# Performance work log

Measured on AMD Instinct MI355X. Metric: run time of the kernel, lower is better.

The kernel has to match this reference:

```python
import jax, jax.numpy as jnp
import numpy as np

NEG_SLOPE = 0.1
NUM_HEADS = 16
ATT0, ATT1 = 64, 64
FOCUS = 3

def lrelu(x):
    return jnp.where(x >= 0, x, NEG_SLOPE * x)

def adaptive_pool_sum(x, a0, a1):
    # adaptive max pool + adaptive avg pool (exact windows since h%a0==0, w%a1==0)
    B, C, h, w = x.shape
    f0, f1 = h // a0, w // a1
    xr = x.reshape(B, C, a0, f0, a1, f1)
    return xr.max(axis=(3, 5)) + xr.mean(axis=(3, 5))

def upsample_bilinear_ac(x, H, W):
    # bilinear upsample with align_corners=True, matching nn.Upsample
    B, C, h, w = x.shape
    def grid(n_out, n_in):
        t = jnp.arange(n_out, dtype=x.dtype) * ((n_in - 1) / (n_out - 1))
        i0 = jnp.clip(jnp.floor(t).astype(jnp.int32), 0, n_in - 2)
        return i0, t - i0.astype(x.dtype)
    y0, wy = grid(H, h)
    x0, wx = grid(W, w)
    wy = wy[None, None, :, None]
    r = x[:, :, y0, :] * (1 - wy) + x[:, :, y0 + 1, :] * wy
    return r[:, :, :, x0] * (1 - wx) + r[:, :, :, x0 + 1] * wx

def _forward(input1, input2, w_in, b_in, w_v, b_v, scale_param, pos1, pos2):
    B, C, W, H = input1.shape
    N = ATT0 * ATT1
    HD = C // NUM_HEADS
    # conv2input: 1x1 conv dim//2 -> dim (channels differ)
    input2 = jnp.einsum('oc,bchw->bohw', w_in, input2) + b_in[None, :, None, None]
    p1 = adaptive_pool_sum(input1, ATT0, ATT1)  # (B,C,64,64)
    p2 = adaptive_pool_sum(input2, ATT0, ATT1)
    q = p1.reshape(B, C, N).transpose(0, 2, 1)  # (B,N,C)
    t2 = p2.reshape(B, C, N).transpose(0, 2, 1)
    q = lrelu(q + pos1)
    k = lrelu(t2 + pos2)
    v = t2
    scale = jax.nn.softplus(scale_param)  # (1,1,C)
    q = q / scale
    k = k / scale
    def focus(t):
        n = jnp.linalg.norm(t, axis=-1, keepdims=True)
        tp = t ** FOCUS
        return n / jnp.linalg.norm(tp, axis=-1, keepdims=True) * tp
    q = focus(q)
    k = focus(k)
    # head split is head-major: C -> (num_heads, head_dim)
    qh = q.reshape(B, N, NUM_HEADS, HD).transpose(0, 2, 1, 3)  # (B,h,N,d)
    kh = k.reshape(B, N, NUM_HEADS, HD).transpose(0, 2, 1, 3)
    vh = v.reshape(B, N, NUM_HEADS, HD).transpose(0, 2, 1, 3)
    # kv-first linear attention: (k^T N^-.5) @ (v N^-.5) = k^T v / N
    kv = jnp.einsum('bhnd,bhne->bhde', kh, vh) / N  # (B,h,d,d)
    x = jnp.einsum('bhnd,bhde->bhne', qh, kv)       # (B,h,N,d)
    x = x.transpose(0, 1, 3, 2).reshape(B, C, N)     # (B,h,d,N) -> (B,C,N)
    # per-head 1x1 conv + leaky relu on v
    v4 = vh.reshape(B * NUM_HEADS, ATT0, ATT1, HD)
    vc = lrelu(jnp.einsum('bxyd,od->boxy', v4, w_v) + b_v[None, :, None, None])
    x = x + vc.reshape(B, C, N)
    attn = x.reshape(B, C, ATT0, ATT1)
    attn = upsample_bilinear_ac(attn, W, H)
    return jax.nn.sigmoid(attn)

def setup_inputs():
    key = jax.random.key(0)
    ks = jax.random.split(key, 6)
    dim, half, hd, N = 512, 256, 32, ATT0 * ATT1
    return {
        'input1': jax.random.normal(ks[0], (8, dim, 128, 128), jnp.float32),
        'input2': jax.random.normal(ks[1], (8, half, 128, 128), jnp.float32),
        'w_in': jax.random.normal(ks[2], (dim, half), jnp.float32) * 0.05,
        'b_in': jnp.zeros((dim,), jnp.float32),
        'w_v': jax.random.normal(ks[3], (hd, hd), jnp.float32) * 0.1,
        'b_v': jnp.zeros((hd,), jnp.float32),
        'scale_param': jnp.zeros((1, 1, dim), jnp.float32),  # nn.Parameter init zeros
        'pos1': jax.random.normal(ks[4], (1, N, dim), jnp.float32) * 0.02,
        'pos2': jax.random.normal(ks[5], (1, N, dim), jnp.float32) * 0.02,
    }

def reference(input1, input2, w_in, b_in, w_v, b_v, scale_param, pos1, pos2):
    return _forward(input1, input2, w_in, b_in, w_v, b_v, scale_param, pos1, pos2)
```

## Files before the change

kernel.cpp:

```cpp
#include <hip/hip_runtime.h>
#include <hip/hip_bf16.h>
#include <math.h>

#define NEG 0.1f

typedef __attribute__((ext_vector_type(8))) short short8;
typedef __attribute__((ext_vector_type(4))) float f32x4;

__device__ __forceinline__ float lrelu(float x){ return x >= 0.f ? x : NEG*x; }

__device__ __forceinline__ unsigned pk2(float lo, float hi){
    __hip_bfloat162 h = __float22bfloat162_rn(make_float2(lo, hi));
    union { __hip_bfloat162 h2; unsigned u; } cv; cv.h2 = h;
    return cv.u;
}
__device__ __forceinline__ float bflo(unsigned u){ return __uint_as_float(u << 16); }
__device__ __forceinline__ float bfhi(unsigned u){ return __uint_as_float(u & 0xFFFF0000u); }

__global__ __launch_bounds__(256) void k_wprep(const float* __restrict__ w_in, unsigned* __restrict__ wbf_u){
    int idx8 = (blockIdx.x*256 + threadIdx.x)*8;
    float4 v0 = *(const float4*)&w_in[idx8];
    float4 v1 = *(const float4*)&w_in[idx8+4];
    uint4 d;
    d.x = pk2(v0.x, v0.y); d.y = pk2(v0.z, v0.w);
    d.z = pk2(v1.x, v1.y); d.w = pk2(v1.z, v1.w);
    *(uint4*)&wbf_u[idx8>>1] = d;
}

__global__ __launch_bounds__(256) void k_pool1(const float* __restrict__ in1, unsigned* __restrict__ p1u){
    const int y = blockIdx.x, cg = blockIdx.y, b = blockIdx.z;
    const int tid = threadIdx.x;
    const int x = tid & 63, w = tid >> 6;
    const int cbase = cg*32 + w*8;
    const float2* iv = (const float2*)in1;
    float out[8];
    #pragma unroll
    for (int j = 0; j < 8; ++j){
        int c = cbase + j;
        size_t r0 = (size_t)(b*512 + c)*8192 + (2*y)*64 + x;
        float2 a = iv[r0];
        float2 bb = iv[r0 + 64];
        float m = fmaxf(fmaxf(a.x,a.y), fmaxf(bb.x,bb.y));
        out[j] = m + (a.x+a.y+bb.x+bb.y)*0.25f;
    }
    uint4 d;
    d.x = pk2(out[0],out[1]); d.y = pk2(out[2],out[3]);
    d.z = pk2(out[4],out[5]); d.w = pk2(out[6],out[7]);
    int n = y*64 + x;
    *(uint4*)&p1u[(size_t)(b*4096 + n)*256 + cg*16 + w*4] = d;
}

__global__ __launch_bounds__(256) void k_convpool(const float* __restrict__ in2, const unsigned* __restrict__ wbf_u,
                                                  const float* __restrict__ b_in, unsigned short* __restrict__ p2t){
    __shared__ unsigned As[128*33];
    __shared__ unsigned Bs[128*32];
    const int b = blockIdx.z, o0 = blockIdx.y*128;
    const int y = blockIdx.x >> 1, xg = blockIdx.x & 1;
    const int tid = threadIdx.x;
    const int lane = tid & 63, w = tid >> 6;
    const int col = lane & 15, q = lane >> 4;

    f32x4 acc[2][8];
    #pragma unroll
    for (int mt=0; mt<2; ++mt)
        #pragma unroll
        for (int nt=0; nt<8; ++nt) acc[mt][nt] = (f32x4){0.f,0.f,0.f,0.f};

    const int a_o8 = tid >> 3;
    const int a_kg = tid & 7;
    const int b_c4 = tid & 15, b_r = (tid>>4)&1, b_kg = tid>>5;
    const int b_n = b_r*64 + b_c4*4;

    for (int kb = 0; kb < 4; ++kb){
        __syncthreads();
        #pragma unroll
        for (int pass=0; pass<4; ++pass){
            int o = pass*32 + a_o8;
            uint4 d = *(const uint4*)&wbf_u[((size_t)(o0+o)*256 + kb*64 + a_kg*8) >> 1];
            *(uint4*)&As[o*32 + ((a_kg ^ ((o>>1)&7))<<2)] = d;
        }
        float r[8][4];
        #pragma unroll
        for (int kk=0; kk<8; ++kk){
            int k = kb*64 + b_kg*8 + kk;
            float4 v = *(const float4*)&in2[((size_t)(b*256 + k)*128 + 2*y + b_r)*128 + xg*64 + b_c4*4];
            r[kk][0]=v.x; r[kk][1]=v.y; r[kk][2]=v.z; r[kk][3]=v.w;
        }
        #pragma unroll
        for (int i=0; i<4; ++i){
            int n = b_n + i;
            uint4 d;
            d.x = pk2(r[0][i], r[1][i]); d.y = pk2(r[2][i], r[3][i]);
            d.z = pk2(r[4][i], r[5][i]); d.w = pk2(r[6][i], r[7][i]);
            *(uint4*)&Bs[n*32 + ((b_kg ^ ((n>>1)&7))<<2)] = d;
        }
        __syncthreads();
        #pragma unroll
        for (int ks=0; ks<2; ++ks){
            int g = ks*4 + q;
            short8 af[2], bf[8];
            #pragma unroll
            for (int mt=0; mt<2; ++mt){
                int m = w*32 + mt*16 + col;
                af[mt] = *(const short8*)&As[m*32 + ((g ^ ((m>>1)&7))<<2)];
            }
            #pragma unroll
            for (int nt=0; nt<8; ++nt){
                int n = nt*16 + col;
                bf[nt] = *(const short8*)&Bs[n*32 + ((g ^ ((n>>1)&7))<<2)];
            }
            #pragma unroll
            for (int mt=0; mt<2; ++mt)
                #pragma unroll
                for (int nt=0; nt<8; ++nt)
                    acc[mt][nt] = __builtin_amdgcn_mfma_f32_16x16x32_bf16(af[mt], bf[nt], acc[mt][nt], 0,0,0);
        }
    }
    __syncthreads();
    float* outs = (float*)As;
    #pragma unroll
    for (int mt=0; mt<2; ++mt){
        #pragma unroll
        for (int nt=0; nt<4; ++nt){
            #pragma unroll
            for (int reg=0; reg<4; ++reg){
                float a = acc[mt][nt][reg], bb = acc[mt][nt+4][reg];
                float mx = fmaxf(a, bb), sm = a + bb;
                float mx2 = fmaxf(mx, __shfl_xor(mx, 1));
                float sm2 = sm + __shfl_xor(sm, 1);
                if ((lane & 1) == 0){
                    int p = nt*8 + (col>>1);
                    int o = w*32 + mt*16 + q*4 + reg;
                    outs[o*33 + p] = mx2 + sm2*0.25f;
                }
            }
        }
    }
    __syncthreads();
    const int o4 = tid & 31, pp = tid >> 5;
    #pragma unroll
    for (int pass=0; pass<4; ++pass){
        int p = pass*8 + pp;
        int n = y*64 + xg*32 + p;
        float v0 = outs[(o4*4+0)*33 + p] + 2.0f*b_in[o0+o4*4+0];
        float v1 = outs[(o4*4+1)*33 + p] + 2.0f*b_in[o0+o4*4+1];
        float v2 = outs[(o4*4+2)*33 + p] + 2.0f*b_in[o0+o4*4+2];
        float v3 = outs[(o4*4+3)*33 + p] + 2.0f*b_in[o0+o4*4+3];
        uint2 d; d.x = pk2(v0,v1); d.y = pk2(v2,v3);
        *(uint2*)&p2t[(size_t)(b*4096 + n)*512 + o0 + o4*4] = d;
    }
}

__global__ __launch_bounds__(256) void k_rows(unsigned* __restrict__ p1u, const unsigned* __restrict__ p2u,
                                              const float* __restrict__ pos1, const float* __restrict__ pos2,
                                              const float* __restrict__ scale_param, unsigned* __restrict__ kfu){
    const int b = blockIdx.y;
    const int tid = threadIdx.x;
    const int half = tid >> 7, t = tid & 127;
    const int n = blockIdx.x*2 + half;
    const int c0 = t*4;
    const size_t base2 = (size_t)(b*4096 + n)*128;
    __shared__ float red[4][4];
    uint2 u1 = *(const uint2*)&p1u[base2*2 + t*2];
    uint2 u2 = *(const uint2*)&p2u[base2*2 + t*2];
    float4 po1 = *(const float4*)&pos1[n*512 + c0];
    float4 po2 = *(const float4*)&pos2[n*512 + c0];
    float4 scv = *(const float4*)&scale_param[c0];
    float qv[4], kv_[4];
    float pq2=0.f, pq6=0.f, pk2_=0.f, pk6=0.f;
    {
        float p1a[4] = {bflo(u1.x), bfhi(u1.x), bflo(u1.y), bfhi(u1.y)};
        float p2a[4] = {bflo(u2.x), bfhi(u2.x), bflo(u2.y), bfhi(u2.y)};
        float poa1[4] = {po1.x,po1.y,po1.z,po1.w};
        float poa2[4] = {po2.x,po2.y,po2.z,po2.w};
        float sca[4] = {scv.x,scv.y,scv.z,scv.w};
        #pragma unroll
        for (int j = 0; j < 4; ++j){
            float sp = sca[j];
            float inv = 1.0f/(fmaxf(sp,0.f) + log1pf(expf(-fabsf(sp))));
            float qq = lrelu(p1a[j] + poa1[j]) * inv;
            float kk = lrelu(p2a[j] + poa2[j]) * inv;
            qv[j]=qq; kv_[j]=kk;
            float a;
            a = qq*qq; pq2 += a; pq6 += a*a*a;
            a = kk*kk; pk2_ += a; pk6 += a*a*a;
        }
    }
    #pragma unroll
    for (int off = 32; off > 0; off >>= 1){
        pq2 += __shfl_xor(pq2, off);
        pq6 += __shfl_xor(pq6, off);
        pk2_ += __shfl_xor(pk2_, off);
        pk6 += __shfl_xor(pk6, off);
    }
    int wave = tid >> 6;
    if ((tid & 63) == 0){ red[wave][0]=pq2; red[wave][1]=pq6; red[wave][2]=pk2_; red[wave][3]=pk6; }
    __syncthreads();
    float sq2 = red[2*half][0]+red[2*half+1][0];
    float sq6 = red[2*half][1]+red[2*half+1][1];
    float sk2 = red[2*half][2]+red[2*half+1][2];
    float sk6 = red[2*half][3]+red[2*half+1][3];
    float fq = sqrtf(sq2/sq6);
    float fk = sqrtf(sk2/sk6);
    uint2 dq, dk;
    dq.x = pk2(qv[0]*qv[0]*qv[0]*fq, qv[1]*qv[1]*qv[1]*fq);
    dq.y = pk2(qv[2]*qv[2]*qv[2]*fq, qv[3]*qv[3]*qv[3]*fq);
    dk.x = pk2(kv_[0]*kv_[0]*kv_[0]*fk, kv_[1]*kv_[1]*kv_[1]*fk);
    dk.y = pk2(kv_[2]*kv_[2]*kv_[2]*fk, kv_[3]*kv_[3]*kv_[3]*fk);
    *(uint2*)&p1u[base2*2 + t*2] = dq;
    *(uint2*)&kfu[base2*2 + t*2] = dk;
}

__global__ __launch_bounds__(256) void k_kv(const unsigned* __restrict__ kfu, const unsigned* __restrict__ p2u,
                                            float* __restrict__ kv){
    __shared__ unsigned ksu[4096], vsu[4096];
    const int nc = blockIdx.x, h = blockIdx.y, b = blockIdx.z;
    const int tid = threadIdx.x;
    #pragma unroll
    for (int it = 0; it < 16; ++it){
        int i = it*256 + tid;
        int n = i >> 4, u = i & 15;
        size_t g = (size_t)(b*4096 + nc*256 + n)*256 + h*16 + u;
        ksu[i] = kfu[g];
        vsu[i] = p2u[g];
    }
    __syncthreads();
    const int d = tid >> 3, e2 = (tid & 7)*2;
    const unsigned kmaskhi = (d & 1) ? 1u : 0u;
    float acc[4] = {0.f,0.f,0.f,0.f};
    #pragma unroll 8
    for (int n = 0; n < 256; ++n){
        unsigned ku = ksu[n*16 + (d>>1)];
        float kd = kmaskhi ? bfhi(ku) : bflo(ku);
        uint2 vv = *(const uint2*)&vsu[n*16 + e2];
        acc[0] += kd*bflo(vv.x); acc[1] += kd*bfhi(vv.x);
        acc[2] += kd*bflo(vv.y); acc[3] += kd*bfhi(vv.y);
    }
    float* dst = &kv[((size_t)(b*16 + h)*32 + d)*32 + (tid&7)*4];
    const float sc = 1.0f/4096.0f;
    atomicAdd(dst+0, acc[0]*sc);
    atomicAdd(dst+1, acc[1]*sc);
    atomicAdd(dst+2, acc[2]*sc);
    atomicAdd(dst+3, acc[3]*sc);
}

__global__ __launch_bounds__(256) void k_attn(const unsigned* __restrict__ qfu, const unsigned* __restrict__ p2u,
                                              const float* __restrict__ kv, const float* __restrict__ w_v,
                                              const float* __restrict__ b_v, unsigned short* __restrict__ attn){
    __shared__ float kvs[1024];
    __shared__ float wvsT[32*36];
    __shared__ float qsl[64*32];
    __shared__ float vsl[64*32];
    __shared__ float to[32*66];
    const int nt = blockIdx.x, h = blockIdx.y, b = blockIdx.z;
    const int tid = threadIdx.x;
    #pragma unroll
    for (int it = 0; it < 4; ++it){
        int i = it*256 + tid;
        kvs[i] = kv[(size_t)(b*16 + h)*1024 + i];
        int e_ = i >> 5, d_ = i & 31;
        wvsT[d_*36 + e_] = w_v[e_*32 + d_];
    }
    #pragma unroll
    for (int it = 0; it < 4; ++it){
        int i = it*256 + tid;
        int nn = i >> 4, cp = i & 15;
        size_t g = (size_t)(b*4096 + nt*64 + nn)*256 + h*16 + cp;
        unsigned qu = qfu[g], vu = p2u[g];
        qsl[nn*32 + cp*2]   = bflo(qu);
        qsl[nn*32 + cp*2+1] = bfhi(qu);
        vsl[nn*32 + cp*2]   = bflo(vu);
        vsl[nn*32 + cp*2+1] = bfhi(vu);
    }
    __syncthreads();
    const int e0 = (tid & 7)*4, ng = tid >> 3;
    float4 bv = make_float4(b_v[e0], b_v[e0+1], b_v[e0+2], b_v[e0+3]);
    #pragma unroll
    for (int half = 0; half < 2; ++half){
        int nn = ng + half*32;
        float xa[4] = {0.f,0.f,0.f,0.f}, va[4] = {0.f,0.f,0.f,0.f};
        #pragma unroll
        for (int dq = 0; dq < 8; ++dq){
            float4 q4 = *(const float4*)&qsl[nn*32 + dq*4];
            float4 v4 = *(const float4*)&vsl[nn*32 + dq*4];
            float qarr[4] = {q4.x,q4.y,q4.z,q4.w};
            float varr[4] = {v4.x,v4.y,v4.z,v4.w};
            #pragma unroll
            for (int l = 0; l < 4; ++l){
                int d = dq*4 + l;
                float4 kvv = *(const float4*)&kvs[d*32 + e0];
                float4 wvv = *(const float4*)&wvsT[d*36 + e0];
                xa[0] += qarr[l]*kvv.x; xa[1] += qarr[l]*kvv.y; xa[2] += qarr[l]*kvv.z; xa[3] += qarr[l]*kvv.w;
                va[0] += varr[l]*wvv.x; va[1] += varr[l]*wvv.y; va[2] += varr[l]*wvv.z; va[3] += varr[l]*wvv.w;
            }
        }
        to[(e0+0)*66 + nn] = xa[0] + lrelu(va[0] + bv.x);
        to[(e0+1)*66 + nn] = xa[1] + lrelu(va[1] + bv.y);
        to[(e0+2)*66 + nn] = xa[2] + lrelu(va[2] + bv.z);
        to[(e0+3)*66 + nn] = xa[3] + lrelu(va[3] + bv.w);
    }
    __syncthreads();
    const int cc = tid >> 3, n0 = (tid & 7)*8;
    uint4 d;
    d.x = pk2(to[cc*66+n0+0], to[cc*66+n0+1]);
    d.y = pk2(to[cc*66+n0+2], to[cc*66+n0+3]);
    d.z = pk2(to[cc*66+n0+4], to[cc*66+n0+5]);
    d.w = pk2(to[cc*66+n0+6], to[cc*66+n0+7]);
    *(uint4*)&attn[((size_t)(b*512) + h*32 + cc)*4096 + nt*64 + n0] = d;
}

__global__ __launch_bounds__(256) void k_up(const unsigned* __restrict__ attn_u, float* __restrict__ out){
    __shared__ float sA[18*65];
    const int qy = blockIdx.x;
    const int bc = blockIdx.y;
    const int tid = threadIdx.x;
    const int ybase = (qy*32*63)/127;
    const size_t sb = (size_t)bc*2048;
    for (int i = tid; i < 576; i += 256){
        int r = i >> 5, cu = i & 31;
        int ridx = ybase + r; if (ridx > 63) ridx = 63;
        unsigned u = attn_u[sb + ridx*32 + cu];
        sA[r*65 + cu*2]   = bflo(u);
        sA[r*65 + cu*2+1] = bfhi(u);
    }
    __syncthreads();
    const float rr = 63.0f/127.0f;
    const int ro = tid >> 3, cbase = tid & 7;
    const int yo = qy*32 + ro;
    float ty = yo * rr;
    int y0 = (int)ty; y0 = y0 > 62 ? 62 : y0;
    float wy = ty - (float)y0;
    const float* ra = &sA[(y0 - ybase)*65];
    const float* rb = ra + 65;
    float* orow = &out[((size_t)bc*128 + yo)*128];
    #pragma unroll
    for (int t = 0; t < 4; ++t){
        int xo0 = (cbase + t*8)*4;
        float4 o;
        float* op = (float*)&o;
        #pragma unroll
        for (int j = 0; j < 4; ++j){
            int xo = xo0 + j;
            float tx = xo * rr;
            int x0 = (int)tx; x0 = x0 > 62 ? 62 : x0;
            float wx = tx - (float)x0;
            float a00 = ra[x0], a01 = ra[x0+1];
            float a10 = rb[x0], a11 = rb[x0+1];
            float v = (a00*(1.f-wy) + a10*wy)*(1.f-wx) + (a01*(1.f-wy) + a11*wy)*wx;
            op[j] = 1.0f/(1.0f + expf(-v));
        }
        *(float4*)&orow[xo0] = o;
    }
}

extern "C" void kernel_launch(void* const* d_in, const int* in_sizes, int n_in,
                              void* d_out, int out_size, void* d_ws, size_t ws_size,
                              hipStream_t stream){
    const float* in1  = (const float*)d_in[0];
    const float* in2  = (const float*)d_in[1];
    const float* w_in = (const float*)d_in[2];
    const float* b_in = (const float*)d_in[3];
    const float* w_v  = (const float*)d_in[4];
    const float* b_v  = (const float*)d_in[5];
    const float* scp  = (const float*)d_in[6];
    const float* pos1 = (const float*)d_in[7];
    const float* pos2 = (const float*)d_in[8];
    float* out = (float*)d_out;
    char* ws  = (char*)d_ws;

    const size_t PBYTES = (size_t)8*4096*512*2;
    unsigned short* p1t  = (unsigned short*)ws;
    unsigned short* p2t  = (unsigned short*)(ws + PBYTES);
    unsigned short* kfoc = (unsigned short*)(ws + 2*PBYTES);
    float*          kvb  = (float*)(ws + 3*PBYTES);
    unsigned*       wbf  = (unsigned*)(ws + 3*PBYTES + (size_t)8*16*32*32*4);

    hipMemsetAsync(kvb, 0, (size_t)8*16*32*32*sizeof(float), stream);
    k_wprep   <<<64,            256, 0, stream>>>(w_in, wbf);
    k_pool1   <<<dim3(64,16,8), 256, 0, stream>>>(in1, (unsigned*)p1t);
    k_convpool<<<dim3(128,4,8), 256, 0, stream>>>(in2, wbf, b_in, p2t);
    k_rows    <<<dim3(2048,8),  256, 0, stream>>>((unsigned*)p1t, (const unsigned*)p2t, pos1, pos2, scp, (unsigned*)kfoc);
    k_kv      <<<dim3(16,16,8), 256, 0, stream>>>((const unsigned*)kfoc, (const unsigned*)p2t, kvb);
    k_attn    <<<dim3(64,16,8), 256, 0, stream>>>((const unsigned*)p1t, (const unsigned*)p2t, kvb, w_v, b_v, kfoc);
    k_up      <<<dim3(4,4096),  256, 0, stream>>>((const unsigned*)kfoc, out);
}
```

Measured before the change: 813.2 us.

## Use MFMA with split-bf16 in attention, register-tile kv, coalesce pool1 stores

k_attn now does the q·kv and v·w_v products with bf16 MFMA instructions. kv and w_v are split into high and low bf16 parts so that precision stays close to fp32 while scalar FMA loops are removed. k_kv gives each thread a 4x4 register tile, spreads the rows across waves, reduces the partials in shared memory, and processes 1024 rows per block. That cuts the number of atomics and the LDS traffic per multiply-add. k_pool1 now stages its outputs in shared memory so the bf16 stores are contiguous, at the cost of an extra barrier.

Result: faster. 742.6 us (-8.7%).

```diff
diff --git a/kernel.cpp b/kernel.cpp
--- a/kernel.cpp
+++ b/kernel.cpp
@@ -16,6 +16,11 @@
 }
 __device__ __forceinline__ float bflo(unsigned u){ return __uint_as_float(u << 16); }
 __device__ __forceinline__ float bfhi(unsigned u){ return __uint_as_float(u & 0xFFFF0000u); }
+
+__device__ __forceinline__ unsigned bfrnd(float f){
+    unsigned u = __float_as_uint(f);
+    return (u + 0x7FFFu + ((u >> 16) & 1u)) & 0xFFFF0000u;
+}
 
 __global__ __launch_bounds__(256) void k_wprep(const float* __restrict__ w_in, unsigned* __restrict__ wbf_u){
     int idx8 = (blockIdx.x*256 + threadIdx.x)*8;
@@ -28,6 +33,7 @@
 }
 
 __global__ __launch_bounds__(256) void k_pool1(const float* __restrict__ in1, unsigned* __restrict__ p1u){
+    __shared__ unsigned sm[64*20];
     const int y = blockIdx.x, cg = blockIdx.y, b = blockIdx.z;
     const int tid = threadIdx.x;
     const int x = tid & 63, w = tid >> 6;
@@ -46,8 +52,11 @@
     uint4 d;
     d.x = pk2(out[0],out[1]); d.y = pk2(out[2],out[3]);
     d.z = pk2(out[4],out[5]); d.w = pk2(out[6],out[7]);
-    int n = y*64 + x;
-    *(uint4*)&p1u[(size_t)(b*4096 + n)*256 + cg*16 + w*4] = d;
+    *(uint4*)&sm[x*20 + w*4] = d;
+    __syncthreads();
+    const int nn = tid >> 2, uq = (tid & 3)*4;
+    uint4 dd = *(const uint4*)&sm[nn*20 + uq];
+    *(uint4*)&p1u[(size_t)(b*4096 + y*64 + nn)*256 + cg*16 + uq] = dd;
 }
 
 __global__ __launch_bounds__(256) void k_convpool(const float* __restrict__ in2, const unsigned* __restrict__ wbf_u,
@@ -214,99 +223,143 @@
 __global__ __launch_bounds__(256) void k_kv(const unsigned* __restrict__ kfu, const unsigned* __restrict__ p2u,
                                             float* __restrict__ kv){
     __shared__ unsigned ksu[4096], vsu[4096];
+    __shared__ float part[4][32*36];
     const int nc = blockIdx.x, h = blockIdx.y, b = blockIdx.z;
     const int tid = threadIdx.x;
-    #pragma unroll
-    for (int it = 0; it < 16; ++it){
-        int i = it*256 + tid;
-        int n = i >> 4, u = i & 15;
-        size_t g = (size_t)(b*4096 + nc*256 + n)*256 + h*16 + u;
-        ksu[i] = kfu[g];
-        vsu[i] = p2u[g];
-    }
-    __syncthreads();
-    const int d = tid >> 3, e2 = (tid & 7)*2;
-    const unsigned kmaskhi = (d & 1) ? 1u : 0u;
-    float acc[4] = {0.f,0.f,0.f,0.f};
-    #pragma unroll 8
-    for (int n = 0; n < 256; ++n){
-        unsigned ku = ksu[n*16 + (d>>1)];
-        float kd = kmaskhi ? bfhi(ku) : bflo(ku);
-        uint2 vv = *(const uint2*)&vsu[n*16 + e2];
-        acc[0] += kd*bflo(vv.x); acc[1] += kd*bfhi(vv.x);
-        acc[2] += kd*bflo(vv.y); acc[3] += kd*bfhi(vv.y);
-    }
-    float* dst = &kv[((size_t)(b*16 + h)*32 + d)*32 + (tid&7)*4];
+    const int wave = tid >> 6, lane = tid & 63;
+    const int d0 = (lane >> 3)*4, e0 = (lane & 7)*4;
+    float acc[4][4];
+    #pragma unroll
+    for (int di=0; di<4; ++di)
+        #pragma unroll
+        for (int ej=0; ej<4; ++ej) acc[di][ej] = 0.f;
+
+    for (int ch = 0; ch < 4; ++ch){
+        __syncthreads();
+        #pragma unroll
+        for (int it = 0; it < 16; ++it){
+            int i = it*256 + tid;
+            int n = i >> 4, u = i & 15;
+            size_t g = (size_t)(b*4096 + nc*1024 + ch*256 + n)*256 + h*16 + u;
+            ksu[i] = kfu[g];
+            vsu[i] = p2u[g];
+        }
+        __syncthreads();
+        #pragma unroll 4
+        for (int i = 0; i < 64; ++i){
+            int n = i*4 + wave;
+            uint2 ku = *(const uint2*)&ksu[n*16 + (d0>>1)];
+            uint2 vu = *(const uint2*)&vsu[n*16 + (e0>>1)];
+            float kd[4] = {bflo(ku.x), bfhi(ku.x), bflo(ku.y), bfhi(ku.y)};
+            float ve[4] = {bflo(vu.x), bfhi(vu.x), bflo(vu.y), bfhi(vu.y)};
+            #pragma unroll
+            for (int di=0; di<4; ++di)
+                #pragma unroll
+                for (int ej=0; ej<4; ++ej)
+                    acc[di][ej] += kd[di]*ve[ej];
+        }
+    }
+    float* pw = &part[wave][0];
+    #pragma unroll
+    for (int di=0; di<4; ++di)
+        *(float4*)&pw[(d0+di)*36 + e0] = make_float4(acc[di][0], acc[di][1], acc[di][2], acc[di][3]);
+    __syncthreads();
+    const int d = tid >> 3, ef = (tid & 7)*4;
+    float4 s0 = *(const float4*)&part[0][d*36 + ef];
+    float4 s1 = *(const float4*)&part[1][d*36 + ef];
+    float4 s2 = *(const float4*)&part[2][d*36 + ef];
+    float4 s3 = *(const float4*)&part[3][d*36 + ef];
     const float sc = 1.0f/4096.0f;
-    atomicAdd(dst+0, acc[0]*sc);
-    atomicAdd(dst+1, acc[1]*sc);
-    atomicAdd(dst+2, acc[2]*sc);
-    atomicAdd(dst+3, acc[3]*sc);
+    float* dst = &kv[((size_t)(b*16 + h)*32 + d)*32 + ef];
+    atomicAdd(dst+0, (s0.x+s1.x+s2.x+s3.x)*sc);
+    atomicAdd(dst+1, (s0.y+s1.y+s2.y+s3.y)*sc);
+    atomicAdd(dst+2, (s0.z+s1.z+s2.z+s3.z)*sc);
+    atomicAdd(dst+3, (s0.w+s1.w+s2.w+s3.w)*sc);
 }
 
 __global__ __launch_bounds__(256) void k_attn(const unsigned* __restrict__ qfu, const unsigned* __restrict__ p2u,
                                               const float* __restrict__ kv, const float* __restrict__ w_v,
                                               const float* __restrict__ b_v, unsigned short* __restrict__ attn){
-    __shared__ float kvs[1024];
-    __shared__ float wvsT[32*36];
-    __shared__ float qsl[64*32];
-    __shared__ float vsl[64*32];
-    __shared__ float to[32*66];
+    __shared__ unsigned short qs[64*40];
+    __shared__ unsigned short vs[64*40];
+    __shared__ unsigned short kvh[32*40], kvl[32*40];
+    __shared__ unsigned short wvh[32*40], wvl[32*40];
+    __shared__ float to[32*68];
     const int nt = blockIdx.x, h = blockIdx.y, b = blockIdx.z;
     const int tid = threadIdx.x;
-    #pragma unroll
-    for (int it = 0; it < 4; ++it){
-        int i = it*256 + tid;
-        kvs[i] = kv[(size_t)(b*16 + h)*1024 + i];
-        int e_ = i >> 5, d_ = i & 31;
-        wvsT[d_*36 + e_] = w_v[e_*32 + d_];
-    }
-    #pragma unroll
-    for (int it = 0; it < 4; ++it){
-        int i = it*256 + tid;
-        int nn = i >> 4, cp = i & 15;
-        size_t g = (size_t)(b*4096 + nt*64 + nn)*256 + h*16 + cp;
-        unsigned qu = qfu[g], vu = p2u[g];
-        qsl[nn*32 + cp*2]   = bflo(qu);
-        qsl[nn*32 + cp*2+1] = bfhi(qu);
-        vsl[nn*32 + cp*2]   = bflo(vu);
-        vsl[nn*32 + cp*2+1] = bfhi(vu);
-    }
-    __syncthreads();
-    const int e0 = (tid & 7)*4, ng = tid >> 3;
-    float4 bv = make_float4(b_v[e0], b_v[e0+1], b_v[e0+2], b_v[e0+3]);
-    #pragma unroll
-    for (int half = 0; half < 2; ++half){
-        int nn = ng + half*32;
-        float xa[4] = {0.f,0.f,0.f,0.f}, va[4] = {0.f,0.f,0.f,0.f};
-        #pragma unroll
-        for (int dq = 0; dq < 8; ++dq){
-            float4 q4 = *(const float4*)&qsl[nn*32 + dq*4];
-            float4 v4 = *(const float4*)&vsl[nn*32 + dq*4];
-            float qarr[4] = {q4.x,q4.y,q4.z,q4.w};
-            float varr[4] = {v4.x,v4.y,v4.z,v4.w};
-            #pragma unroll
-            for (int l = 0; l < 4; ++l){
-                int d = dq*4 + l;
-                float4 kvv = *(const float4*)&kvs[d*32 + e0];
-                float4 wvv = *(const float4*)&wvsT[d*36 + e0];
-                xa[0] += qarr[l]*kvv.x; xa[1] += qarr[l]*kvv.y; xa[2] += qarr[l]*kvv.z; xa[3] += qarr[l]*kvv.w;
-                va[0] += varr[l]*wvv.x; va[1] += varr[l]*wvv.y; va[2] += varr[l]*wvv.z; va[3] += varr[l]*wvv.w;
-            }
-        }
-        to[(e0+0)*66 + nn] = xa[0] + lrelu(va[0] + bv.x);
-        to[(e0+1)*66 + nn] = xa[1] + lrelu(va[1] + bv.y);
-        to[(e0+2)*66 + nn] = xa[2] + lrelu(va[2] + bv.z);
-        to[(e0+3)*66 + nn] = xa[3] + lrelu(va[3] + bv.w);
-    }
-    __syncthreads();
-    const int cc = tid >> 3, n0 = (tid & 7)*8;
+    {
+        const int nn = tid >> 2, up = (tid & 3)*4;
+        size_t g = (size_t)(b*4096 + nt*64 + nn)*256 + h*16 + up;
+        uint4 qu = *(const uint4*)&qfu[g];
+        uint4 vu = *(const uint4*)&p2u[g];
+        *(uint4*)&qs[nn*40 + up*2] = qu;
+        *(uint4*)&vs[nn*40 + up*2] = vu;
+    }
+    {
+        const int e = tid >> 3, d0 = (tid & 7)*4;
+        const float* kvp = &kv[(size_t)(b*16 + h)*1024];
+        unsigned hb[4]; float lo[4];
+        #pragma unroll
+        for (int i=0; i<4; ++i){
+            float f = kvp[(d0+i)*32 + e];
+            hb[i] = bfrnd(f);
+            lo[i] = f - __uint_as_float(hb[i]);
+        }
+        uint2 dh, dl;
+        dh.x = (hb[0]>>16) | hb[1]; dh.y = (hb[2]>>16) | hb[3];
+        dl.x = pk2(lo[0], lo[1]);   dl.y = pk2(lo[2], lo[3]);
+        *(uint2*)&kvh[e*40 + d0] = dh;
+        *(uint2*)&kvl[e*40 + d0] = dl;
+        float4 wf = *(const float4*)&w_v[e*32 + d0];
+        float wfa[4] = {wf.x, wf.y, wf.z, wf.w};
+        #pragma unroll
+        for (int i=0; i<4; ++i){
+            hb[i] = bfrnd(wfa[i]);
+            lo[i] = wfa[i] - __uint_as_float(hb[i]);
+        }
+        dh.x = (hb[0]>>16) | hb[1]; dh.y = (hb[2]>>16) | hb[3];
+        dl.x = pk2(lo[0], lo[1]);   dl.y = pk2(lo[2], lo[3]);
+        *(uint2*)&wvh[e*40 + d0] = dh;
+        *(uint2*)&wvl[e*40 + d0] = dl;
+    }
+    __syncthreads();
+    const int lane = tid & 63, w = tid >> 6;
+    const int col = lane & 15, q8 = lane >> 4;
+    short8 aq = *(const short8*)&qs[(w*16 + col)*40 + q8*8];
+    short8 av = *(const short8*)&vs[(w*16 + col)*40 + q8*8];
+    f32x4 ax[2], avc[2];
+    #pragma unroll
+    for (int et=0; et<2; ++et){ ax[et] = (f32x4){0.f,0.f,0.f,0.f}; avc[et] = (f32x4){0.f,0.f,0.f,0.f}; }
+    #pragma unroll
+    for (int et=0; et<2; ++et){
+        short8 bh = *(const short8*)&kvh[(et*16 + col)*40 + q8*8];
+        short8 bl = *(const short8*)&kvl[(et*16 + col)*40 + q8*8];
+        ax[et] = __builtin_amdgcn_mfma_f32_16x16x32_bf16(aq, bh, ax[et], 0,0,0);
+        ax[et] = __builtin_amdgcn_mfma_f32_16x16x32_bf16(aq, bl, ax[et], 0,0,0);
+        short8 wh = *(const short8*)&wvh[(et*16 + col)*40 + q8*8];
+        short8 wl = *(const short8*)&wvl[(et*16 + col)*40 + q8*8];
+        avc[et] = __builtin_amdgcn_mfma_f32_16x16x32_bf16(av, wh, avc[et], 0,0,0);
+        avc[et] = __builtin_amdgcn_mfma_f32_16x16x32_bf16(av, wl, avc[et], 0,0,0);
+    }
+    #pragma unroll
+    for (int et=0; et<2; ++et){
+        int e = et*16 + col;
+        float bve = b_v[e];
+        float4 o;
+        o.x = ax[et][0] + lrelu(avc[et][0] + bve);
+        o.y = ax[et][1] + lrelu(avc[et][1] + bve);
+        o.z = ax[et][2] + lrelu(avc[et][2] + bve);
+        o.w = ax[et][3] + lrelu(avc[et][3] + bve);
+        *(float4*)&to[e*68 + w*16 + q8*4] = o;
+    }
+    __syncthreads();
+    const int cc = tid >> 3, n8 = (tid & 7)*8;
+    float4 t0 = *(const float4*)&to[cc*68 + n8];
+    float4 t1 = *(const float4*)&to[cc*68 + n8 + 4];
     uint4 d;
-    d.x = pk2(to[cc*66+n0+0], to[cc*66+n0+1]);
-    d.y = pk2(to[cc*66+n0+2], to[cc*66+n0+3]);
-    d.z = pk2(to[cc*66+n0+4], to[cc*66+n0+5]);
-    d.w = pk2(to[cc*66+n0+6], to[cc*66+n0+7]);
-    *(uint4*)&attn[((size_t)(b*512) + h*32 + cc)*4096 + nt*64 + n0] = d;
+    d.x = pk2(t0.x,t0.y); d.y = pk2(t0.z,t0.w);
+    d.z = pk2(t1.x,t1.y); d.w = pk2(t1.z,t1.w);
+    *(uint4*)&attn[((size_t)(b*512) + h*32 + cc)*4096 + nt*64 + n8] = d;
 }
 
 __global__ __launch_bounds__(256) void k_up(const unsigned* __restrict__ attn_u, float* __restrict__ out){
@@ -380,7 +433,7 @@
     k_pool1   <<<dim3(64,16,8), 256, 0, stream>>>(in1, (unsigned*)p1t);
     k_convpool<<<dim3(128,4,8), 256, 0, stream>>>(in2, wbf, b_in, p2t);
     k_rows    <<<dim3(2048,8),  256, 0, stream>>>((unsigned*)p1t, (const unsigned*)p2t, pos1, pos2, scp, (unsigned*)kfoc);
-    k_kv      <<<dim3(16,16,8), 256, 0, stream>>>((const unsigned*)kfoc, (const unsigned*)p2t, kvb);
+    k_kv      <<<dim3(4,16,8),  256, 0, stream>>>((const unsigned*)kfoc, (const unsigned*)p2t, kvb);
     k_attn    <<<dim3(64,16,8), 256, 0, stream>>>((const unsigned*)p1t, (const unsigned*)p2t, kvb, w_v, b_v, kfoc);
     k_up      <<<dim3(4,4096),  256, 0, stream>>>((const unsigned*)kfoc, out);
 }
```
